# Optimization experiments

Hardware: AMD Instinct MI355X
Metric: run time of the kernel (lower is better)

## Reference

```python
import jax, jax.numpy as jnp
import numpy as np

B, K, VDIM, QDIM, NHID, SE_INNER = 8192, 6, 2048, 1024, 1024, 128

def setup_inputs() -> dict:
    key = jax.random.key(0)
    ks = jax.random.split(key, 10)
    w = lambda k, shape: jax.random.normal(k, shape, dtype=jnp.float32) * 0.02
    return {
        "v": jax.random.normal(ks[0], (B, K, VDIM), dtype=jnp.float32),
        "q": jax.random.normal(ks[1], (B, QDIM), dtype=jnp.float32),
        "mask": (jax.random.uniform(ks[2], (B, K)) > 0.5).astype(jnp.float32),
        "W1": w(ks[3], (NHID, VDIM + QDIM)),   # FCNet weight-normed Linear (effective weight)
        "b1": jnp.zeros((NHID,), jnp.float32),
        "Wl": w(ks[4], (1, NHID)),             # logits Linear(num_hid, 1)
        "bl": jnp.zeros((1,), jnp.float32),
        "Wse1": w(ks[5], (SE_INNER, 1)),       # SELayer fc1, no bias
        "Wse2": w(ks[6], (1, SE_INNER)),       # SELayer fc2, no bias
        "Wf": w(ks[7], (VDIM, 1)),             # final_att_proj Linear(1, v_dim)
        "bf": jnp.zeros((VDIM,), jnp.float32),
    }

def reference(v, q, mask, W1, b1, Wl, bl, Wse1, Wse2, Wf, bf):
    Bn, Kn, _ = v.shape
    # logits(v, q): concat q to every object, FCNet (Linear+ReLU), Linear->1 (dropout is identity at eval)
    qe = jnp.broadcast_to(q[:, None, :], (Bn, Kn, q.shape[-1]))
    vq = jnp.concatenate([v, qe], axis=-1)                       # [B,K,vd+qd]
    joint = jax.nn.relu(jnp.einsum('bkf,hf->bkh', vq, W1) + b1)  # [B,K,NHID]
    logits = jnp.einsum('bkh,oh->bko', joint, Wl) + bl           # [B,K,1]
    single_att = jax.nn.softmax(logits, axis=1)
    w = logits                                                   # view(mask_b, 6, -1) is identity here
    w_ctx = w * mask[..., None]                                  # [B,K,1]
    # per-role sum over the 5 complementary roles == total - self (exact complement index sets)
    neigh = jnp.sum(w_ctx, axis=1, keepdims=True) - w_ctx        # [B,K,1]
    x = neigh[..., None]                                         # [B,K,1,1]
    # SE gate: FC(1->128) -> ReLU -> FC(128->1) -> Sigmoid; out = x * (1 - y)
    y = jax.nn.sigmoid(jax.nn.relu(x @ Wse1.T) @ Wse2.T)          # [B,K,1,1]
    gated = x * (1.0 - y)
    # final_att_proj(gated + w[:,role].unsqueeze(-1)) : Linear(1 -> v_dim)
    upd = (gated + w[..., None]) @ Wf.T + bf                     # [B,K,1,VDIM]
    context_erased_att = upd.reshape(Bn * Kn, 1, upd.shape[-1])  # [B*K,1,VDIM]
    return single_att, context_erased_att
```

## Files before the change

### kernel.cpp

```cpp
#include <hip/hip_runtime.h>

#define B_SZ   8192
#define KOBJ   6
#define VD     2048
#define QD     1024
#define NHID_  1024
#define SEIN   128
#define M_TOT  (B_SZ * KOBJ)
#define K_TOT  (VD + QD)

typedef __bf16 bf16x8 __attribute__((ext_vector_type(8)));
typedef float  f32x4  __attribute__((ext_vector_type(4)));
typedef unsigned int uint4v __attribute__((ext_vector_type(4)));

__device__ __forceinline__ unsigned short f2bf(float f) {
    unsigned u = __builtin_bit_cast(unsigned, f);
    u += 0x7fffu + ((u >> 16) & 1u);
    return (unsigned short)(u >> 16);
}

__global__ __launch_bounds__(256) void conv_bf16(const float* __restrict__ src,
                                                 unsigned short* __restrict__ dst,
                                                 int n8) {
    int i = blockIdx.x * 256 + threadIdx.x;
    if (i < n8) {
        float4 f0 = ((const float4*)src)[2 * i];
        float4 f1 = ((const float4*)src)[2 * i + 1];
        uint4v d;
        d[0] = (unsigned)f2bf(f0.x) | ((unsigned)f2bf(f0.y) << 16);
        d[1] = (unsigned)f2bf(f0.z) | ((unsigned)f2bf(f0.w) << 16);
        d[2] = (unsigned)f2bf(f1.x) | ((unsigned)f2bf(f1.y) << 16);
        d[3] = (unsigned)f2bf(f1.z) | ((unsigned)f2bf(f1.w) << 16);
        ((uint4v*)dst)[i] = d;
    }
}

__global__ __launch_bounds__(256) void gemm_logits(
    const unsigned short* __restrict__ vb, const unsigned short* __restrict__ qb,
    const unsigned short* __restrict__ W1b,
    const float* __restrict__ b1, const float* __restrict__ Wl,
    float* __restrict__ logits)
{
    __shared__ unsigned short At[128 * 32];
    __shared__ unsigned short Bt[128 * 32];

    const int tid  = threadIdx.x;
    const int bid  = blockIdx.x;
    const int nb   = bid & 7;
    const int mb   = bid >> 3;
    const int m0   = mb * 128;
    const int n0   = nb * 128;
    const int wave = tid >> 6, lane = tid & 63;
    const int quad = lane >> 4, l16 = lane & 15;
    const int wr   = (wave >> 1) * 64, wc = (wave & 1) * 64;

    int rowA[2], chA[2];
    const unsigned short* gav[2];
    const unsigned short* gaq[2];
    const unsigned short* gb[2];
    unsigned short* ldsA[2];
    unsigned short* ldsB[2];
    #pragma unroll
    for (int c = 0; c < 2; ++c) {
        int seg = wave * 2 + c;
        rowA[c] = seg * 16 + (lane >> 2);
        chA[c]  = (lane & 3) ^ ((rowA[c] >> 1) & 3);
        int m   = m0 + rowA[c];
        gav[c]  = vb + (size_t)m * VD + chA[c] * 8;
        gaq[c]  = qb + (size_t)(m / KOBJ) * QD + chA[c] * 8;
        gb[c]   = W1b + (size_t)(n0 + rowA[c]) * K_TOT + chA[c] * 8;
        ldsA[c] = &At[seg * 512];
        ldsB[c] = &Bt[seg * 512];
    }

    f32x4 acc[4][4] = {};
    const int swz = (l16 >> 1) & 3;

    for (int kk = 0; kk < K_TOT; kk += 32) {
        __syncthreads();
        const bool isq = (kk >= VD);
        #pragma unroll
        for (int c = 0; c < 2; ++c) {
            const unsigned short* g = isq ? (gaq[c] + (kk - VD)) : (gav[c] + kk);
            __builtin_amdgcn_global_load_lds(
                (const __attribute__((address_space(1))) void*)g,
                (__attribute__((address_space(3))) void*)ldsA[c], 16, 0, 0);
        }
        #pragma unroll
        for (int c = 0; c < 2; ++c) {
            const unsigned short* g = gb[c] + kk;
            __builtin_amdgcn_global_load_lds(
                (const __attribute__((address_space(1))) void*)g,
                (__attribute__((address_space(3))) void*)ldsB[c], 16, 0, 0);
        }
        __syncthreads();

        bf16x8 af[4], bfr[4];
        #pragma unroll
        for (int i = 0; i < 4; ++i)
            af[i] = __builtin_bit_cast(bf16x8,
                *(const uint4v*)&At[(wr + i * 16 + l16) * 32 + ((quad ^ swz) * 8)]);
        #pragma unroll
        for (int j = 0; j < 4; ++j)
            bfr[j] = __builtin_bit_cast(bf16x8,
                *(const uint4v*)&Bt[(wc + j * 16 + l16) * 32 + ((quad ^ swz) * 8)]);
        #pragma unroll
        for (int i = 0; i < 4; ++i)
            #pragma unroll
            for (int j = 0; j < 4; ++j)
                acc[i][j] = __builtin_amdgcn_mfma_f32_16x16x32_bf16(af[i], bfr[j], acc[i][j], 0, 0, 0);
    }

    #pragma unroll
    for (int i = 0; i < 4; ++i) {
        #pragma unroll
        for (int r = 0; r < 4; ++r) {
            int m = m0 + wr + i * 16 + quad * 4 + r;
            float sum = 0.f;
            #pragma unroll
            for (int j = 0; j < 4; ++j) {
                int n = n0 + wc + j * 16 + l16;
                float h = fmaxf(acc[i][j][r] + b1[n], 0.f);
                sum = fmaf(h, Wl[n], sum);
            }
            sum += __shfl_xor(sum, 1);
            sum += __shfl_xor(sum, 2);
            sum += __shfl_xor(sum, 4);
            sum += __shfl_xor(sum, 8);
            if (l16 == 0) atomicAdd(&logits[m], sum);
        }
    }
}

__global__ __launch_bounds__(256) void se_kernel(
    const float* __restrict__ logits, const float* __restrict__ mask,
    const float* __restrict__ bl,
    const float* __restrict__ Wse1, const float* __restrict__ Wse2,
    float* __restrict__ out_att, float* __restrict__ s_buf)
{
    int b = blockIdx.x * 256 + threadIdx.x;
    if (b >= B_SZ) return;
    float w[KOBJ];
    float blv = bl[0];
    #pragma unroll
    for (int k = 0; k < KOBJ; ++k) w[k] = logits[b * KOBJ + k] + blv;

    float mx = w[0];
    #pragma unroll
    for (int k = 1; k < KOBJ; ++k) mx = fmaxf(mx, w[k]);
    float e[KOBJ], den = 0.f;
    #pragma unroll
    for (int k = 0; k < KOBJ; ++k) { e[k] = __expf(w[k] - mx); den += e[k]; }
    float rden = 1.f / den;
    #pragma unroll
    for (int k = 0; k < KOBJ; ++k) out_att[b * KOBJ + k] = e[k] * rden;

    float wcm[KOBJ], tot = 0.f;
    #pragma unroll
    for (int k = 0; k < KOBJ; ++k) { wcm[k] = w[k] * mask[b * KOBJ + k]; tot += wcm[k]; }

    #pragma unroll
    for (int k = 0; k < KOBJ; ++k) {
        float x = tot - wcm[k];
        float a = 0.f;
        for (int i = 0; i < SEIN; ++i)
            a = fmaf(fmaxf(x * Wse1[i], 0.f), Wse2[i], a);
        float y = 1.f / (1.f + __expf(-a));
        s_buf[b * KOBJ + k] = x * (1.f - y) + w[k];
    }
}

__global__ __launch_bounds__(256) void out_writer(
    const float* __restrict__ s_buf, const float* __restrict__ Wf,
    const float* __restrict__ bfv, float* __restrict__ out)
{
    int m = blockIdx.x;
    float s = s_buf[m];
    const float4* wf4 = (const float4*)Wf;
    const float4* bf4 = (const float4*)bfv;
    float4* o4 = (float4*)(out + (size_t)m * VD);
    #pragma unroll
    for (int it = 0; it < VD / 4 / 256; ++it) {
        int t = threadIdx.x + it * 256;
        float4 wv = wf4[t], bv = bf4[t];
        float4 r;
        r.x = fmaf(s, wv.x, bv.x);
        r.y = fmaf(s, wv.y, bv.y);
        r.z = fmaf(s, wv.z, bv.z);
        r.w = fmaf(s, wv.w, bv.w);
        o4[t] = r;
    }
}

extern "C" void kernel_launch(void* const* d_in, const int* in_sizes, int n_in,
                              void* d_out, int out_size, void* d_ws, size_t ws_size,
                              hipStream_t stream) {
    const float* v    = (const float*)d_in[0];
    const float* q    = (const float*)d_in[1];
    const float* mask = (const float*)d_in[2];
    const float* W1   = (const float*)d_in[3];
    const float* b1   = (const float*)d_in[4];
    const float* Wl   = (const float*)d_in[5];
    const float* bl   = (const float*)d_in[6];
    const float* Wse1 = (const float*)d_in[7];
    const float* Wse2 = (const float*)d_in[8];
    const float* Wf   = (const float*)d_in[9];
    const float* bfv  = (const float*)d_in[10];
    float* out = (float*)d_out;

    char* ws = (char*)d_ws;
    unsigned short* W1b = (unsigned short*)ws;
    float* logits = (float*)(ws + 6291456);
    float* s_buf  = (float*)(ws + 6291456 + 196608);

    unsigned short* vb = (unsigned short*)((char*)d_out + (size_t)M_TOT * 4);
    unsigned short* qb = (unsigned short*)((char*)d_out + (size_t)M_TOT * 4 + 201326592);

    hipMemsetAsync(logits, 0, M_TOT * sizeof(float), stream);
    conv_bf16<<<(NHID_ * K_TOT / 8 + 255) / 256, 256, 0, stream>>>(W1, W1b, NHID_ * K_TOT / 8);
    conv_bf16<<<(M_TOT * VD / 8 + 255) / 256, 256, 0, stream>>>(v, vb, M_TOT * VD / 8);
    conv_bf16<<<(B_SZ * QD / 8 + 255) / 256, 256, 0, stream>>>(q, qb, B_SZ * QD / 8);
    gemm_logits<<<(M_TOT / 128) * (NHID_ / 128), 256, 0, stream>>>(vb, qb, W1b, b1, Wl, logits);
    se_kernel<<<(B_SZ + 255) / 256, 256, 0, stream>>>(logits, mask, bl, Wse1, Wse2, out, s_buf);
    out_writer<<<M_TOT, 256, 0, stream>>>(s_buf, Wf, bfv, out + M_TOT);
}
```

Measured before the change: 1.094 ms.

## Factor query projection out of per-object GEMM and reuse across objects

Splits the concatenated [v,q] GEMM into a small per-batch q·W1q GEMM (with bias folded in) stored as fp32, and a v·W1v GEMM over the 2048-wide v dimension whose epilogue adds the precomputed q contribution before ReLU. This removes the redundant recomputation of the q projection for each of the 6 objects, reducing GEMM FLOPs by about a third of the K dimension. It adds an extra kernel, a 32MB fp32 intermediate stored in scratch space in the output buffer, and extra gathered reads in the epilogue.

```diff
diff --git a/kernel.cpp b/kernel.cpp
--- a/kernel.cpp
+++ b/kernel.cpp
@@ -35,11 +35,9 @@
     }
 }
 
-__global__ __launch_bounds__(256) void gemm_logits(
-    const unsigned short* __restrict__ vb, const unsigned short* __restrict__ qb,
-    const unsigned short* __restrict__ W1b,
-    const float* __restrict__ b1, const float* __restrict__ Wl,
-    float* __restrict__ logits)
+__global__ __launch_bounds__(256) void gemm_q(
+    const unsigned short* __restrict__ qb, const unsigned short* __restrict__ W1b,
+    const float* __restrict__ b1, float* __restrict__ Gq)
 {
     __shared__ unsigned short At[128 * 32];
     __shared__ unsigned short Bt[128 * 32];
@@ -54,21 +52,17 @@
     const int quad = lane >> 4, l16 = lane & 15;
     const int wr   = (wave >> 1) * 64, wc = (wave & 1) * 64;
 
-    int rowA[2], chA[2];
-    const unsigned short* gav[2];
-    const unsigned short* gaq[2];
+    const unsigned short* ga[2];
     const unsigned short* gb[2];
     unsigned short* ldsA[2];
     unsigned short* ldsB[2];
     #pragma unroll
     for (int c = 0; c < 2; ++c) {
         int seg = wave * 2 + c;
-        rowA[c] = seg * 16 + (lane >> 2);
-        chA[c]  = (lane & 3) ^ ((rowA[c] >> 1) & 3);
-        int m   = m0 + rowA[c];
-        gav[c]  = vb + (size_t)m * VD + chA[c] * 8;
-        gaq[c]  = qb + (size_t)(m / KOBJ) * QD + chA[c] * 8;
-        gb[c]   = W1b + (size_t)(n0 + rowA[c]) * K_TOT + chA[c] * 8;
+        int row = seg * 16 + (lane >> 2);
+        int ch  = (lane & 3) ^ ((row >> 1) & 3);
+        ga[c]   = qb + (size_t)(m0 + row) * QD + ch * 8;
+        gb[c]   = W1b + (size_t)(n0 + row) * K_TOT + VD + ch * 8;
         ldsA[c] = &At[seg * 512];
         ldsB[c] = &Bt[seg * 512];
     }
@@ -76,23 +70,18 @@
     f32x4 acc[4][4] = {};
     const int swz = (l16 >> 1) & 3;
 
-    for (int kk = 0; kk < K_TOT; kk += 32) {
-        __syncthreads();
-        const bool isq = (kk >= VD);
-        #pragma unroll
-        for (int c = 0; c < 2; ++c) {
-            const unsigned short* g = isq ? (gaq[c] + (kk - VD)) : (gav[c] + kk);
-            __builtin_amdgcn_global_load_lds(
-                (const __attribute__((address_space(1))) void*)g,
+    for (int kk = 0; kk < QD; kk += 32) {
+        __syncthreads();
+        #pragma unroll
+        for (int c = 0; c < 2; ++c)
+            __builtin_amdgcn_global_load_lds(
+                (const __attribute__((address_space(1))) void*)(ga[c] + kk),
                 (__attribute__((address_space(3))) void*)ldsA[c], 16, 0, 0);
-        }
-        #pragma unroll
-        for (int c = 0; c < 2; ++c) {
-            const unsigned short* g = gb[c] + kk;
-            __builtin_amdgcn_global_load_lds(
-                (const __attribute__((address_space(1))) void*)g,
+        #pragma unroll
+        for (int c = 0; c < 2; ++c)
+            __builtin_amdgcn_global_load_lds(
+                (const __attribute__((address_space(1))) void*)(gb[c] + kk),
                 (__attribute__((address_space(3))) void*)ldsB[c], 16, 0, 0);
-        }
         __syncthreads();
 
         bf16x8 af[4], bfr[4];
@@ -112,15 +101,96 @@
     }
 
     #pragma unroll
+    for (int i = 0; i < 4; ++i)
+        #pragma unroll
+        for (int j = 0; j < 4; ++j) {
+            int n = n0 + wc + j * 16 + l16;
+            float bv = b1[n];
+            #pragma unroll
+            for (int r = 0; r < 4; ++r) {
+                int m = m0 + wr + i * 16 + quad * 4 + r;
+                Gq[(size_t)m * NHID_ + n] = acc[i][j][r] + bv;
+            }
+        }
+}
+
+__global__ __launch_bounds__(256) void gemm_logits(
+    const unsigned short* __restrict__ vb, const unsigned short* __restrict__ W1b,
+    const float* __restrict__ Gq, const float* __restrict__ Wl,
+    float* __restrict__ logits)
+{
+    __shared__ unsigned short At[128 * 32];
+    __shared__ unsigned short Bt[128 * 32];
+
+    const int tid  = threadIdx.x;
+    const int bid  = blockIdx.x;
+    const int nb   = bid & 7;
+    const int mb   = bid >> 3;
+    const int m0   = mb * 128;
+    const int n0   = nb * 128;
+    const int wave = tid >> 6, lane = tid & 63;
+    const int quad = lane >> 4, l16 = lane & 15;
+    const int wr   = (wave >> 1) * 64, wc = (wave & 1) * 64;
+
+    const unsigned short* gav[2];
+    const unsigned short* gb[2];
+    unsigned short* ldsA[2];
+    unsigned short* ldsB[2];
+    #pragma unroll
+    for (int c = 0; c < 2; ++c) {
+        int seg = wave * 2 + c;
+        int row = seg * 16 + (lane >> 2);
+        int ch  = (lane & 3) ^ ((row >> 1) & 3);
+        gav[c]  = vb + (size_t)(m0 + row) * VD + ch * 8;
+        gb[c]   = W1b + (size_t)(n0 + row) * K_TOT + ch * 8;
+        ldsA[c] = &At[seg * 512];
+        ldsB[c] = &Bt[seg * 512];
+    }
+
+    f32x4 acc[4][4] = {};
+    const int swz = (l16 >> 1) & 3;
+
+    for (int kk = 0; kk < VD; kk += 32) {
+        __syncthreads();
+        #pragma unroll
+        for (int c = 0; c < 2; ++c)
+            __builtin_amdgcn_global_load_lds(
+                (const __attribute__((address_space(1))) void*)(gav[c] + kk),
+                (__attribute__((address_space(3))) void*)ldsA[c], 16, 0, 0);
+        #pragma unroll
+        for (int c = 0; c < 2; ++c)
+            __builtin_amdgcn_global_load_lds(
+                (const __attribute__((address_space(1))) void*)(gb[c] + kk),
+                (__attribute__((address_space(3))) void*)ldsB[c], 16, 0, 0);
+        __syncthreads();
+
+        bf16x8 af[4], bfr[4];
+        #pragma unroll
+        for (int i = 0; i < 4; ++i)
+            af[i] = __builtin_bit_cast(bf16x8,
+                *(const uint4v*)&At[(wr + i * 16 + l16) * 32 + ((quad ^ swz) * 8)]);
+        #pragma unroll
+        for (int j = 0; j < 4; ++j)
+            bfr[j] = __builtin_bit_cast(bf16x8,
+                *(const uint4v*)&Bt[(wc + j * 16 + l16) * 32 + ((quad ^ swz) * 8)]);
+        #pragma unroll
+        for (int i = 0; i < 4; ++i)
+            #pragma unroll
+            for (int j = 0; j < 4; ++j)
+                acc[i][j] = __builtin_amdgcn_mfma_f32_16x16x32_bf16(af[i], bfr[j], acc[i][j], 0, 0, 0);
+    }
+
+    #pragma unroll
     for (int i = 0; i < 4; ++i) {
         #pragma unroll
         for (int r = 0; r < 4; ++r) {
             int m = m0 + wr + i * 16 + quad * 4 + r;
+            const float* gqr = Gq + (size_t)(m / KOBJ) * NHID_;
             float sum = 0.f;
             #pragma unroll
             for (int j = 0; j < 4; ++j) {
                 int n = n0 + wc + j * 16 + l16;
-                float h = fmaxf(acc[i][j][r] + b1[n], 0.f);
+                float h = fmaxf(acc[i][j][r] + gqr[n], 0.f);
                 sum = fmaf(h, Wl[n], sum);
             }
             sum += __shfl_xor(sum, 1);
@@ -215,12 +285,14 @@
 
     unsigned short* vb = (unsigned short*)((char*)d_out + (size_t)M_TOT * 4);
     unsigned short* qb = (unsigned short*)((char*)d_out + (size_t)M_TOT * 4 + 201326592);
+    float* Gq = (float*)((char*)d_out + (size_t)M_TOT * 4 + 201326592 + 16777216);
 
     hipMemsetAsync(logits, 0, M_TOT * sizeof(float), stream);
     conv_bf16<<<(NHID_ * K_TOT / 8 + 255) / 256, 256, 0, stream>>>(W1, W1b, NHID_ * K_TOT / 8);
+    conv_bf16<<<(B_SZ * QD / 8 + 255) / 256, 256, 0, stream>>>(q, qb, B_SZ * QD / 8);
+    gemm_q<<<(B_SZ / 128) * (NHID_ / 128), 256, 0, stream>>>(qb, W1b, b1, Gq);
     conv_bf16<<<(M_TOT * VD / 8 + 255) / 256, 256, 0, stream>>>(v, vb, M_TOT * VD / 8);
-    conv_bf16<<<(B_SZ * QD / 8 + 255) / 256, 256, 0, stream>>>(q, qb, B_SZ * QD / 8);
-    gemm_logits<<<(M_TOT / 128) * (NHID_ / 128), 256, 0, stream>>>(vb, qb, W1b, b1, Wl, logits);
+    gemm_logits<<<(M_TOT / 128) * (NHID_ / 128), 256, 0, stream>>>(vb, W1b, Gq, Wl, logits);
     se_kernel<<<(B_SZ + 255) / 256, 256, 0, stream>>>(logits, mask, bl, Wse1, Wse2, out, s_buf);
     out_writer<<<M_TOT, 256, 0, stream>>>(s_buf, Wf, bfv, out + M_TOT);
 }
```

Result: faster. 1.062 ms (-2.9%).
